# Performance work log

Hardware: AMD Instinct MI355X
Metric: run time of the kernel (lower is better)

The kernel has to match this reference:

```python
import jax, jax.numpy as jnp
import numpy as np

B, S, HID, H, D = 4, 1024, 1024, 16, 64
MAXP = 1024  # max_position_embeddings
EPS = 1e-8


def setup_inputs() -> dict:
    key = jax.random.key(0)
    ks = jax.random.split(key, 9)
    scale = 0.02  # keep logits small since masked_softmax has no max-subtraction
    return {
        "hidden_states": jax.random.normal(ks[0], (B, S, HID), jnp.float32),
        "attention_mask": jnp.zeros((B, 1, 1, S), jnp.float32),
        "skim_mask": jax.random.randint(ks[1], (B, S), 0, 2, jnp.int32),
        "Wq": jax.random.normal(ks[2], (HID, HID), jnp.float32) * scale,
        "bq": jnp.zeros((HID,), jnp.float32),
        "Wk": jax.random.normal(ks[3], (HID, HID), jnp.float32) * scale,
        "bk": jnp.zeros((HID,), jnp.float32),
        "Wv": jax.random.normal(ks[4], (HID, HID), jnp.float32) * scale,
        "bv": jnp.zeros((HID,), jnp.float32),
        "dist_emb": jax.random.normal(ks[5], (2 * MAXP - 1, D), jnp.float32) * scale,
    }


def reference(hidden_states, attention_mask, skim_mask, Wq, bq, Wk, bk, Wv, bv, dist_emb):
    # Linear projections (W stored as [in, out]) then split heads: [B,H,S,D]
    def heads(x):
        return x.reshape(B, S, H, D).transpose(0, 2, 1, 3)

    q = heads(hidden_states @ Wq + bq)
    k = heads(hidden_states @ Wk + bk)
    v = heads(hidden_states @ Wv + bv)

    # raw scores [B,H,S,S]
    scores = jnp.einsum('bhld,bhrd->bhlr', q, k)

    # relative_key positional bias
    pos = jnp.arange(S)
    distance = pos[:, None] - pos[None, :]                 # [S,S]
    pe = dist_emb[distance + MAXP - 1]                     # [S,S,D]
    scores = scores + jnp.einsum('bhld,lrd->bhlr', q, pe)

    scores = scores / jnp.sqrt(jnp.float32(D))
    scores = scores + attention_mask

    # skim_mask branch: masked_softmax (exp * mask, normalized with eps)
    mask = skim_mask[:, None, None, :].astype(scores.dtype)  # [B,1,1,S]
    exps = jnp.exp(scores) * mask
    probs = exps / (EPS + exps.sum(-1, keepdims=True))
    # dropout in eval mode -> identity

    ctx = jnp.einsum('bhlr,bhrd->bhld', probs, v)
    return ctx.transpose(0, 2, 1, 3).reshape(B, S, HID)
```

## Files before the change

### kernel.cpp

```cpp
#include <hip/hip_runtime.h>
#include <hip/hip_bf16.h>


#define EPSV 1e-8f

typedef short bfrag __attribute__((ext_vector_type(8)));
typedef float cfrag __attribute__((ext_vector_type(16)));

__device__ __forceinline__ short f2bf(float f) {
    __hip_bfloat16 h = __float2bfloat16(f);
    return *reinterpret_cast<short*>(&h);
}
__device__ __forceinline__ float bf2f(short s) {
    unsigned int u = ((unsigned int)(unsigned short)s) << 16;
    return __builtin_bit_cast(float, u);
}
__device__ __forceinline__ unsigned int pk2(short a, short b) {
    return (unsigned int)(unsigned short)a | ((unsigned int)(unsigned short)b << 16);
}

__global__ __launch_bounds__(256) void prep(
    const float* __restrict__ hidden, const float* __restrict__ Wq,
    const float* __restrict__ Wk, const float* __restrict__ Wv,
    const float* __restrict__ dist,
    short* __restrict__ Xs, short* __restrict__ Wt, short* __restrict__ Db)
{
    __shared__ short Tl[32 * 72];
    const int bid = blockIdx.x, tid = threadIdx.x;

    if (bid < 2048) {
        const int mt = bid >> 4, kg = bid & 15;
        const int m_l = tid >> 3, k8 = (tid & 7) * 8;
        const float* src = hidden + (size_t)(mt * 32 + m_l) * 1024 + kg * 64 + k8;
        float4 v0 = *(const float4*)src, v1 = *(const float4*)(src + 4);
        short o[8];
        o[0] = f2bf(v0.x); o[1] = f2bf(v0.y); o[2] = f2bf(v0.z); o[3] = f2bf(v0.w);
        o[4] = f2bf(v1.x); o[5] = f2bf(v1.y); o[6] = f2bf(v1.z); o[7] = f2bf(v1.w);
        *(bfrag*)&Tl[m_l * 72 + k8] = *(bfrag*)o;
        __syncthreads();
        const int l31 = tid & 31, q2 = (tid >> 5) & 1, kc = tid >> 6;
        bfrag r = *(const bfrag*)&Tl[l31 * 72 + kc * 16 + q2 * 8];
        *(bfrag*)(Xs + ((size_t)(mt * 64 + kg * 4 + kc) * 64 + q2 * 32 + l31) * 8) = r;
    } else if (bid < 3584) {
        const int t = bid - 2048, z = t >> 9, nt = (t >> 4) & 31, kg = t & 15;
        const float* W = (z == 0) ? Wq : ((z == 1) ? Wk : Wv);
        const int k_l = tid >> 2, n8 = (tid & 3) * 8;
        const float* src = W + (size_t)(kg * 64 + k_l) * 1024 + nt * 32 + n8;
        float4 v0 = *(const float4*)src, v1 = *(const float4*)(src + 4);
        float vv[8] = {v0.x, v0.y, v0.z, v0.w, v1.x, v1.y, v1.z, v1.w};
#pragma unroll
        for (int i = 0; i < 8; i++)
            Tl[(n8 + i) * 72 + k_l] = f2bf(vv[i]);
        __syncthreads();
        const int l31 = tid & 31, q2 = (tid >> 5) & 1, kc = tid >> 6;
        bfrag r = *(const bfrag*)&Tl[l31 * 72 + kc * 16 + q2 * 8];
        *(bfrag*)(Wt + (size_t)z * 1048576
                  + ((size_t)(nt * 64 + kg * 4 + kc) * 64 + q2 * 32 + l31) * 8) = r;
    } else {
        const int idx = (bid - 3584) * 256 + tid;
        if (idx < 16376) {
            const float* src = dist + (size_t)idx * 8;
            float4 v0 = *(const float4*)src, v1 = *(const float4*)(src + 4);
            short o[8];
            o[0] = f2bf(v0.x); o[1] = f2bf(v0.y); o[2] = f2bf(v0.z); o[3] = f2bf(v0.w);
            o[4] = f2bf(v1.x); o[5] = f2bf(v1.y); o[6] = f2bf(v1.z); o[7] = f2bf(v1.w);
            *(bfrag*)(Db + (size_t)idx * 8) = *(bfrag*)o;
        }
    }
}

__global__ __launch_bounds__(256) void qkv_mfma(
    const short* __restrict__ Xs, const short* __restrict__ Wt,
    const float* __restrict__ bq, const float* __restrict__ bk,
    const float* __restrict__ bv,
    short* __restrict__ Qf, short* __restrict__ Kf, short* __restrict__ Vt)
{
    const int z = blockIdx.z;
    const short* W = Wt + (size_t)z * 1048576;
    const float* bias = (z == 0) ? bq : ((z == 1) ? bk : bv);
    const float scale = (z == 0) ? 0.125f : 1.0f;

    const int tid = threadIdx.x, lane = tid & 63, wid = tid >> 6;
    const int q2 = lane >> 5, l31 = lane & 31;
    const int wr = wid >> 1, wc = wid & 1;
    const int m0 = blockIdx.x * 128, n0 = blockIdx.y * 128;

    cfrag acc[2][2];
#pragma unroll
    for (int i = 0; i < 2; i++)
#pragma unroll
        for (int j = 0; j < 2; j++)
#pragma unroll
            for (int e = 0; e < 16; e++) acc[i][j][e] = 0.f;

    const short* ap0 = Xs + ((size_t)((m0 >> 5) + wr * 2 + 0) * 64 * 64 + lane) * 8;
    const short* ap1 = Xs + ((size_t)((m0 >> 5) + wr * 2 + 1) * 64 * 64 + lane) * 8;
    const short* bp0 = W  + ((size_t)((n0 >> 5) + wc * 2 + 0) * 64 * 64 + lane) * 8;
    const short* bp1 = W  + ((size_t)((n0 >> 5) + wc * 2 + 1) * 64 * 64 + lane) * 8;

#pragma unroll 4
    for (int kc = 0; kc < 64; kc++) {
        const int off = kc * 512;
        bfrag a0 = *(const bfrag*)(ap0 + off);
        bfrag a1 = *(const bfrag*)(ap1 + off);
        bfrag b0 = *(const bfrag*)(bp0 + off);
        bfrag b1 = *(const bfrag*)(bp1 + off);
        acc[0][0] = __builtin_amdgcn_mfma_f32_32x32x16_bf16(a0, b0, acc[0][0], 0, 0, 0);
        acc[0][1] = __builtin_amdgcn_mfma_f32_32x32x16_bf16(a0, b1, acc[0][1], 0, 0, 0);
        acc[1][0] = __builtin_amdgcn_mfma_f32_32x32x16_bf16(a1, b0, acc[1][0], 0, 0, 0);
        acc[1][1] = __builtin_amdgcn_mfma_f32_32x32x16_bf16(a1, b1, acc[1][1], 0, 0, 0);
    }

#pragma unroll
    for (int nt = 0; nt < 2; nt++) {
        const int c = n0 + wc * 64 + nt * 32 + l31;
        const float bval = bias[c];
        const int h = c >> 6;
        const int d = nt * 32 + l31;
#pragma unroll
        for (int mt = 0; mt < 2; mt++) {
            const int tok0 = m0 + wr * 64 + mt * 32;
            const int bb = tok0 >> 10, s_base = tok0 & 1023;
            const size_t bhbase = (size_t)(bb * 16 + h) * 65536;
            if (z < 2) {
                short* outp = (z == 0) ? Qf : Kf;
                const size_t fbase = bhbase
                    + ((size_t)((s_base >> 5) * 4 + (d >> 4)) * 64
                       + ((d >> 3) & 1) * 32) * 8 + (d & 7);
#pragma unroll
                for (int reg = 0; reg < 16; reg++) {
                    const int row = (reg & 3) + 8 * (reg >> 2) + 4 * q2;
                    outp[fbase + (size_t)row * 8] = f2bf((acc[mt][nt][reg] + bval) * scale);
                }
            } else {
#pragma unroll
                for (int g = 0; g < 4; g++) {
                    const float e0 = acc[mt][nt][4 * g + 0] + bval;
                    const float e1 = acc[mt][nt][4 * g + 1] + bval;
                    const float e2 = acc[mt][nt][4 * g + 2] + bval;
                    const float e3 = acc[mt][nt][4 * g + 3] + bval;
                    uint2 w2;
                    w2.x = pk2(f2bf(e0), f2bf(e1));
                    w2.y = pk2(f2bf(e2), f2bf(e3));
                    const size_t flat = bhbase
                        + ((size_t)(nt * 64 + (s_base >> 4) + (g >> 1)) * 64
                           + (g & 1) * 32 + l31) * 8 + 4 * q2;
                    *(uint2*)(Vt + flat) = w2;
                }
            }
        }
    }
}

__global__ __launch_bounds__(256) void attn_mfma(
    const short* __restrict__ Qf, const short* __restrict__ Kf,
    const short* __restrict__ Vt, const short* __restrict__ Db,
    const float* __restrict__ amask, const int* __restrict__ skim,
    float* __restrict__ out)
{
    __shared__ short Tb[128 * 132];
    __shared__ short Es[4][32 * 72];
    __shared__ float Lg[1024];

    const int tid = threadIdx.x, lane = tid & 63, w = tid >> 6;
    const int q2 = lane >> 5, l31 = lane & 31;
    const int h2 = w >> 1;
    const int bh = blockIdx.x, b = bh >> 4, hh = bh & 15;
    const int l0 = blockIdx.y * 128;

    {
        const int r4 = tid * 4;
        float4 am = *(const float4*)(amask + b * 1024 + r4);
        int4 sk = *(const int4*)(skim + b * 1024 + r4);
        Lg[r4 + 0] = __expf(am.x) * (float)sk.x;
        Lg[r4 + 1] = __expf(am.y) * (float)sk.y;
        Lg[r4 + 2] = __expf(am.z) * (float)sk.z;
        Lg[r4 + 3] = __expf(am.w) * (float)sk.w;
    }
    __syncthreads();

    const short* Qg = Qf + (size_t)bh * 65536;
    const short* Kg = Kf + (size_t)bh * 65536;
    const short* Vg = Vt + (size_t)bh * 65536;

    bfrag qa[4];
#pragma unroll
    for (int c = 0; c < 4; c++)
        qa[c] = *(const bfrag*)(Qg + ((size_t)(((l0 >> 5) + w) * 4 + c) * 64 + lane) * 8);

    cfrag oacc[2];
#pragma unroll
    for (int mt = 0; mt < 2; mt++)
#pragma unroll
        for (int e = 0; e < 16; e++) oacc[mt][e] = 0.f;
    float esum = 0.f;

    const int lrow = 32 * w + l31;

    for (int r0 = -64; r0 < 1024; r0 += 64) {
        const int bd = l0 - r0 - 64 + 64 * h2;
#pragma unroll
        for (int mt = 0; mt < 2; mt++) {
            cfrag t;
#pragma unroll
            for (int e = 0; e < 16; e++) t[e] = 0.f;
            const int drow = bd + 32 * mt + l31;
            const int er = min(max(drow + 1023, 0), 2046);
#pragma unroll
            for (int kc = 0; kc < 4; kc++) {
                bfrag pb = *(const bfrag*)(Db + (size_t)er * 64 + kc * 16 + q2 * 8);
                t = __builtin_amdgcn_mfma_f32_32x32x16_bf16(pb, qa[kc], t, 0, 0, 0);
            }
#pragma unroll
            for (int g = 0; g < 4; g++) {
                const int slot = (bd + 32 * mt + 8 * g + 4 * q2) & 127;
                uint2 w2;
                w2.x = pk2(f2bf(t[4 * g + 0]), f2bf(t[4 * g + 1]));
                w2.y = pk2(f2bf(t[4 * g + 2]), f2bf(t[4 * g + 3]));
                *(uint2*)&Tb[lrow * 132 + slot] = w2;
            }
        }
        if (r0 < 0) continue;

        cfrag sfr[2];
#pragma unroll
        for (int mt = 0; mt < 2; mt++) {
#pragma unroll
            for (int e = 0; e < 16; e++) sfr[mt][e] = 0.f;
#pragma unroll
            for (int kc = 0; kc < 4; kc++) {
                bfrag kb = *(const bfrag*)(Kg
                    + ((size_t)(((r0 >> 5) + mt) * 4 + kc) * 64 + lane) * 8);
                sfr[mt] = __builtin_amdgcn_mfma_f32_32x32x16_bf16(
                    kb, qa[kc], sfr[mt], 0, 0, 0);
            }
        }

        const int lg = l0 + 32 * w + l31;
#pragma unroll
        for (int mt = 0; mt < 2; mt++) {
#pragma unroll
            for (int g = 0; g < 4; g++) {
                const int rb = r0 + 32 * mt + 8 * g + 4 * q2;
                float4 g4 = *(const float4*)&Lg[rb];
                short s4[4];
#pragma unroll
                for (int j = 0; j < 4; j++) {
                    const int dist = lg - (rb + j);
                    const float tv = bf2f(Tb[lrow * 132 + (dist & 127)]);
                    const float gv = (j == 0) ? g4.x : (j == 1) ? g4.y
                                   : (j == 2) ? g4.z : g4.w;
                    const float e = __expf(sfr[mt][4 * g + j] + tv) * gv;
                    s4[j] = f2bf(e);
                    esum += bf2f(s4[j]);
                }
                uint2 w2;
                w2.x = pk2(s4[0], s4[1]);
                w2.y = pk2(s4[2], s4[3]);
                *(uint2*)&Es[w][l31 * 72 + 32 * mt + 8 * g + 4 * q2] = w2;
            }
        }

#pragma unroll
        for (int kc = 0; kc < 4; kc++) {
            bfrag ef = *(const bfrag*)&Es[w][l31 * 72 + kc * 16 + q2 * 8];
#pragma unroll
            for (int mtd = 0; mtd < 2; mtd++) {
                bfrag vb = *(const bfrag*)(Vg
                    + ((size_t)(mtd * 64 + (r0 >> 4) + kc) * 64 + lane) * 8);
                oacc[mtd] = __builtin_amdgcn_mfma_f32_32x32x16_bf16(
                    vb, ef, oacc[mtd], 0, 0, 0);
            }
        }
    }

    const float den = EPSV + esum + __shfl_xor(esum, 32);
    const float inv = 1.0f / den;
    const int lg = l0 + 32 * w + l31;
    float* ob = out + ((size_t)(b * 1024 + lg) * 1024) + hh * 64;
#pragma unroll
    for (int mtd = 0; mtd < 2; mtd++) {
#pragma unroll
        for (int g = 0; g < 4; g++) {
            float4 o;
            o.x = oacc[mtd][4 * g + 0] * inv;
            o.y = oacc[mtd][4 * g + 1] * inv;
            o.z = oacc[mtd][4 * g + 2] * inv;
            o.w = oacc[mtd][4 * g + 3] * inv;
            *(float4*)(ob + 32 * mtd + 8 * g + 4 * q2) = o;
        }
    }
}

extern "C" void kernel_launch(void* const* d_in, const int* in_sizes, int n_in,
                              void* d_out, int out_size, void* d_ws, size_t ws_size,
                              hipStream_t stream) {
    const float* hidden = (const float*)d_in[0];
    const float* amask  = (const float*)d_in[1];
    const int*   skim   = (const int*)d_in[2];
    const float* Wq     = (const float*)d_in[3];
    const float* bq     = (const float*)d_in[4];
    const float* Wk     = (const float*)d_in[5];
    const float* bk     = (const float*)d_in[6];
    const float* Wv     = (const float*)d_in[7];
    const float* bv     = (const float*)d_in[8];
    const float* dist   = (const float*)d_in[9];
    float* out = (float*)d_out;

    char* w = (char*)d_ws;
    short* Xs  = (short*)(w);
    short* Wt  = (short*)(w + ((size_t)8 << 20));
    short* Db  = (short*)(w + ((size_t)14 << 20));
    short* Qf  = (short*)(w + ((size_t)15 << 20));
    short* Kf  = (short*)(w + ((size_t)23 << 20));
    short* Vt  = (short*)(w + ((size_t)31 << 20));

    prep<<<3648, 256, 0, stream>>>(hidden, Wq, Wk, Wv, dist, Xs, Wt, Db);
    qkv_mfma<<<dim3(32, 8, 3), 256, 0, stream>>>(Xs, Wt, bq, bk, bv, Qf, Kf, Vt);
    attn_mfma<<<dim3(64, 8), 256, 0, stream>>>(Qf, Kf, Vt, Db, amask, skim, out);
}
```

Baseline: 199.3 us.

## Stage QKV GEMM tiles via LDS and split attention key range across waves

```diff
diff --git a/kernel.cpp b/kernel.cpp
--- a/kernel.cpp
+++ b/kernel.cpp
@@ -17,6 +17,11 @@
 }
 __device__ __forceinline__ unsigned int pk2(short a, short b) {
     return (unsigned int)(unsigned short)a | ((unsigned int)(unsigned short)b << 16);
+}
+__device__ __forceinline__ void gl2lds16(const void* g, void* l) {
+    __builtin_amdgcn_global_load_lds(
+        (const __attribute__((address_space(1))) unsigned int*)g,
+        (__attribute__((address_space(3))) unsigned int*)l, 16, 0, 0);
 }
 
 __global__ __launch_bounds__(256) void prep(
@@ -75,8 +80,12 @@
     const float* __restrict__ bv,
     short* __restrict__ Qf, short* __restrict__ Kf, short* __restrict__ Vt)
 {
+    __shared__ short As[8192];
+    __shared__ short Bs[8192];
+
     const int z = blockIdx.z;
-    const short* W = Wt + (size_t)z * 1048576;
+    const char* Xb = (const char*)Xs;
+    const char* Wb = (const char*)(Wt + (size_t)z * 1048576);
     const float* bias = (z == 0) ? bq : ((z == 1) ? bk : bv);
     const float scale = (z == 0) ? 0.125f : 1.0f;
 
@@ -93,22 +102,35 @@
 #pragma unroll
             for (int e = 0; e < 16; e++) acc[i][j][e] = 0.f;
 
-    const short* ap0 = Xs + ((size_t)((m0 >> 5) + wr * 2 + 0) * 64 * 64 + lane) * 8;
-    const short* ap1 = Xs + ((size_t)((m0 >> 5) + wr * 2 + 1) * 64 * 64 + lane) * 8;
-    const short* bp0 = W  + ((size_t)((n0 >> 5) + wc * 2 + 0) * 64 * 64 + lane) * 8;
-    const short* bp1 = W  + ((size_t)((n0 >> 5) + wc * 2 + 1) * 64 * 64 + lane) * 8;
-
-#pragma unroll 4
-    for (int kc = 0; kc < 64; kc++) {
-        const int off = kc * 512;
-        bfrag a0 = *(const bfrag*)(ap0 + off);
-        bfrag a1 = *(const bfrag*)(ap1 + off);
-        bfrag b0 = *(const bfrag*)(bp0 + off);
-        bfrag b1 = *(const bfrag*)(bp1 + off);
-        acc[0][0] = __builtin_amdgcn_mfma_f32_32x32x16_bf16(a0, b0, acc[0][0], 0, 0, 0);
-        acc[0][1] = __builtin_amdgcn_mfma_f32_32x32x16_bf16(a0, b1, acc[0][1], 0, 0, 0);
-        acc[1][0] = __builtin_amdgcn_mfma_f32_32x32x16_bf16(a1, b0, acc[1][0], 0, 0, 0);
-        acc[1][1] = __builtin_amdgcn_mfma_f32_32x32x16_bf16(a1, b1, acc[1][1], 0, 0, 0);
+    for (int kg = 0; kg < 16; kg++) {
+        __syncthreads();
+        const size_t abase = ((size_t)(((m0 >> 5) + wid) * 16 + kg)) * 4096;
+        const size_t bbase = ((size_t)(((n0 >> 5) + wid) * 16 + kg)) * 4096;
+#pragma unroll
+        for (int i = 0; i < 4; i++) {
+            gl2lds16(Xb + abase + i * 1024 + lane * 16,
+                     (char*)As + wid * 4096 + i * 1024);
+            gl2lds16(Wb + bbase + i * 1024 + lane * 16,
+                     (char*)Bs + wid * 4096 + i * 1024);
+        }
+        __syncthreads();
+
+        bfrag a[2][4], b[2][4];
+#pragma unroll
+        for (int i = 0; i < 2; i++)
+#pragma unroll
+            for (int kc = 0; kc < 4; kc++) {
+                a[i][kc] = *(const bfrag*)&As[((2 * wr + i) * 4 + kc) * 512 + lane * 8];
+                b[i][kc] = *(const bfrag*)&Bs[((2 * wc + i) * 4 + kc) * 512 + lane * 8];
+            }
+#pragma unroll
+        for (int kc = 0; kc < 4; kc++)
+#pragma unroll
+            for (int mt = 0; mt < 2; mt++)
+#pragma unroll
+                for (int nt = 0; nt < 2; nt++)
+                    acc[mt][nt] = __builtin_amdgcn_mfma_f32_32x32x16_bf16(
+                        a[mt][kc], b[nt][kc], acc[mt][nt], 0, 0, 0);
     }
 
 #pragma unroll
@@ -159,14 +181,14 @@
     float* __restrict__ out)
 {
     __shared__ short Tb[128 * 132];
-    __shared__ short Es[4][32 * 72];
     __shared__ float Lg[1024];
+    __shared__ float EsumL[2][64];
 
     const int tid = threadIdx.x, lane = tid & 63, w = tid >> 6;
     const int q2 = lane >> 5, l31 = lane & 31;
-    const int h2 = w >> 1;
+    const int lw = w & 1, rw = w >> 1;
     const int bh = blockIdx.x, b = bh >> 4, hh = bh & 15;
-    const int l0 = blockIdx.y * 128;
+    const int l0 = blockIdx.y * 64;
 
     {
         const int r4 = tid * 4;
@@ -186,7 +208,7 @@
     bfrag qa[4];
 #pragma unroll
     for (int c = 0; c < 4; c++)
-        qa[c] = *(const bfrag*)(Qg + ((size_t)(((l0 >> 5) + w) * 4 + c) * 64 + lane) * 8);
+        qa[c] = *(const bfrag*)(Qg + ((size_t)(((l0 >> 5) + lw) * 4 + c) * 64 + lane) * 8);
 
     cfrag oacc[2];
 #pragma unroll
@@ -196,9 +218,11 @@
     float esum = 0.f;
 
     const int lrow = 32 * w + l31;
-
-    for (int r0 = -64; r0 < 1024; r0 += 64) {
-        const int bd = l0 - r0 - 64 + 64 * h2;
+    const int L = l0 + 32 * lw;
+    const int lgl = L + l31;
+    const int r0s = rw * 512;
+
+    auto Tcompute = [&](int bd) {
 #pragma unroll
         for (int mt = 0; mt < 2; mt++) {
             cfrag t;
@@ -220,7 +244,13 @@
                 *(uint2*)&Tb[lrow * 132 + slot] = w2;
             }
         }
-        if (r0 < 0) continue;
+    };
+
+    Tcompute(L - r0s);
+
+    for (int rt = 0; rt < 8; rt++) {
+        const int r0 = r0s + rt * 64;
+        Tcompute(L - r0 - 64);
 
         cfrag sfr[2];
 #pragma unroll
@@ -236,7 +266,7 @@
             }
         }
 
-        const int lg = l0 + 32 * w + l31;
+        unsigned int P[2][8];
 #pragma unroll
         for (int mt = 0; mt < 2; mt++) {
 #pragma unroll
@@ -246,7 +276,7 @@
                 short s4[4];
 #pragma unroll
                 for (int j = 0; j < 4; j++) {
-                    const int dist = lg - (rb + j);
+                    const int dist = lgl - (rb + j);
                     const float tv = bf2f(Tb[lrow * 132 + (dist & 127)]);
                     const float gv = (j == 0) ? g4.x : (j == 1) ? g4.y
                                    : (j == 2) ? g4.z : g4.w;
@@ -254,40 +284,64 @@
                     s4[j] = f2bf(e);
                     esum += bf2f(s4[j]);
                 }
-                uint2 w2;
-                w2.x = pk2(s4[0], s4[1]);
-                w2.y = pk2(s4[2], s4[3]);
-                *(uint2*)&Es[w][l31 * 72 + 32 * mt + 8 * g + 4 * q2] = w2;
+                P[mt][2 * g + 0] = pk2(s4[0], s4[1]);
+                P[mt][2 * g + 1] = pk2(s4[2], s4[3]);
             }
         }
 
 #pragma unroll
         for (int kc = 0; kc < 4; kc++) {
-            bfrag ef = *(const bfrag*)&Es[w][l31 * 72 + kc * 16 + q2 * 8];
+            const int a = 4 * (kc & 1), mt = kc >> 1;
+            const unsigned int x0 = __shfl_xor((int)P[mt][a + 0], 32);
+            const unsigned int x1 = __shfl_xor((int)P[mt][a + 1], 32);
+            const unsigned int x2 = __shfl_xor((int)P[mt][a + 2], 32);
+            const unsigned int x3 = __shfl_xor((int)P[mt][a + 3], 32);
+            union { unsigned int u[4]; bfrag f; } ef;
+            ef.u[0] = q2 ? x2 : P[mt][a + 0];
+            ef.u[1] = q2 ? x3 : P[mt][a + 1];
+            ef.u[2] = q2 ? P[mt][a + 2] : x0;
+            ef.u[3] = q2 ? P[mt][a + 3] : x1;
 #pragma unroll
             for (int mtd = 0; mtd < 2; mtd++) {
                 bfrag vb = *(const bfrag*)(Vg
                     + ((size_t)(mtd * 64 + (r0 >> 4) + kc) * 64 + lane) * 8);
                 oacc[mtd] = __builtin_amdgcn_mfma_f32_32x32x16_bf16(
-                    vb, ef, oacc[mtd], 0, 0, 0);
-            }
-        }
-    }
-
-    const float den = EPSV + esum + __shfl_xor(esum, 32);
-    const float inv = 1.0f / den;
-    const int lg = l0 + 32 * w + l31;
-    float* ob = out + ((size_t)(b * 1024 + lg) * 1024) + hh * 64;
-#pragma unroll
-    for (int mtd = 0; mtd < 2; mtd++) {
-#pragma unroll
-        for (int g = 0; g < 4; g++) {
-            float4 o;
-            o.x = oacc[mtd][4 * g + 0] * inv;
-            o.y = oacc[mtd][4 * g + 1] * inv;
-            o.z = oacc[mtd][4 * g + 2] * inv;
-            o.w = oacc[mtd][4 * g + 3] * inv;
-            *(float4*)(ob + 32 * mtd + 8 * g + 4 * q2) = o;
+                    vb, ef.f, oacc[mtd], 0, 0, 0);
+            }
+        }
+    }
+
+    const float es2 = esum + __shfl_xor(esum, 32);
+    if (q2 == 0) EsumL[rw][32 * lw + l31] = es2;
+    __syncthreads();
+
+    float* Osc = (float*)Tb;
+    if (rw == 1) {
+#pragma unroll
+        for (int mtd = 0; mtd < 2; mtd++)
+#pragma unroll
+            for (int reg = 0; reg < 16; reg++) {
+                const int d = 32 * mtd + (reg & 3) + 8 * (reg >> 2) + 4 * q2;
+                Osc[d * 68 + 32 * lw + l31] = oacc[mtd][reg];
+            }
+    }
+    __syncthreads();
+    if (rw == 0) {
+        const float den = EPSV + EsumL[0][32 * lw + l31] + EsumL[1][32 * lw + l31];
+        const float inv = 1.0f / den;
+        float* ob = out + ((size_t)(b * 1024 + lgl) * 1024) + hh * 64;
+#pragma unroll
+        for (int mtd = 0; mtd < 2; mtd++) {
+#pragma unroll
+            for (int g = 0; g < 4; g++) {
+                const int db = 32 * mtd + 8 * g + 4 * q2;
+                float4 o;
+                o.x = (oacc[mtd][4 * g + 0] + Osc[(db + 0) * 68 + 32 * lw + l31]) * inv;
+                o.y = (oacc[mtd][4 * g + 1] + Osc[(db + 1) * 68 + 32 * lw + l31]) * inv;
+                o.z = (oacc[mtd][4 * g + 2] + Osc[(db + 2) * 68 + 32 * lw + l31]) * inv;
+                o.w = (oacc[mtd][4 * g + 3] + Osc[(db + 3) * 68 + 32 * lw + l31]) * inv;
+                *(float4*)(ob + db) = o;
+            }
         }
     }
 }
@@ -317,5 +371,5 @@
 
     prep<<<3648, 256, 0, stream>>>(hidden, Wq, Wk, Wv, dist, Xs, Wt, Db);
     qkv_mfma<<<dim3(32, 8, 3), 256, 0, stream>>>(Xs, Wt, bq, bk, bv, Qf, Kf, Vt);
-    attn_mfma<<<dim3(64, 8), 256, 0, stream>>>(Qf, Kf, Vt, Db, amask, skim, out);
-}
+    attn_mfma<<<dim3(64, 16), 256, 0, stream>>>(Qf, Kf, Vt, Db, amask, skim, out);
+}
```

Result: slower. 241.1 us (+21.0%).
